# Performance work log

Measured on AMD Instinct MI355X. Metric: run time of the kernel, lower is better.

The kernel has to match this reference:

```python
import jax, jax.numpy as jnp
import numpy as np

N_HEADS = 16
ROPE_THETA = 10000.0


def setup_inputs() -> dict:
    B, T, C = 4, 2048, 2048
    hd = C // N_HEADS  # 128
    key = jax.random.key(0)
    k1, k2, k3 = jax.random.split(key, 3)
    x = jax.random.normal(k1, (B, T, C), dtype=jnp.float32)
    # RoPE frequencies: angle[t, j] = t / theta^(2j/hd)
    inv_freq = 1.0 / (ROPE_THETA ** (jnp.arange(0, hd, 2, dtype=jnp.float32) / hd))  # (hd/2,)
    angles = jnp.arange(T, dtype=jnp.float32)[:, None] * inv_freq[None, :]  # (T, hd/2)
    freqs_cos = jnp.cos(angles)
    freqs_sin = jnp.sin(angles)
    W_qkv = jax.random.normal(k2, (C, 3 * C), dtype=jnp.float32) * (C ** -0.5)
    W_out = jax.random.normal(k3, (C, C), dtype=jnp.float32) * (C ** -0.5)
    return {"x": x, "freqs_cos": freqs_cos, "freqs_sin": freqs_sin, "W_qkv": W_qkv, "W_out": W_out}


def _apply_rope(t, cos, sin):
    # t: (B, H, T, hd); cos/sin: (T, hd/2). Interleaved-pair rotation, matching
    # torch view_as_complex on reshape(..., hd/2, 2).
    hd = t.shape[-1]
    tr = t.reshape(*t.shape[:-1], hd // 2, 2)
    x0, x1 = tr[..., 0], tr[..., 1]  # (B, H, T, hd/2)
    o0 = x0 * cos - x1 * sin
    o1 = x0 * sin + x1 * cos
    return jnp.stack([o0, o1], axis=-1).reshape(t.shape)


def reference(x, freqs_cos, freqs_sin, W_qkv, W_out):
    B, T, C = x.shape
    H = N_HEADS
    hd = C // H
    qkv = x @ W_qkv  # (B, T, 3C)
    q, k, v = jnp.split(qkv, 3, axis=-1)

    def heads(t):
        return t.reshape(B, T, H, hd).transpose(0, 2, 1, 3)  # (B, H, T, hd)

    cos, sin = freqs_cos[:T], freqs_sin[:T]
    q = _apply_rope(heads(q), cos, sin)
    k = _apply_rope(heads(k), cos, sin)
    v = heads(v)

    scale = hd ** -0.5
    scores = jnp.einsum('bhqd,bhkd->bhqk', q, k) * scale  # (B, H, T, T)
    causal = jnp.tril(jnp.ones((T, T), dtype=bool))
    scores = jnp.where(causal, scores, jnp.finfo(scores.dtype).min)
    attn = jax.nn.softmax(scores, axis=-1)
    out = jnp.einsum('bhqk,bhkd->bhqd', attn, v)  # (B, H, T, hd)
    out = out.transpose(0, 2, 1, 3).reshape(B, T, C)
    return out @ W_out, k, v
```

## Files before the change

kernel.cpp:

```cpp
#include <hip/hip_runtime.h>
#include <cstdint>
#include <cstddef>

typedef __attribute__((ext_vector_type(8))) short bf16x8;
typedef __attribute__((ext_vector_type(4))) float f32x4;

__device__ __forceinline__ unsigned short f2bf(float f) {
  union { float f; unsigned u; } v; v.f = f;
  unsigned r = v.u + 0x7FFFu + ((v.u >> 16) & 1u);
  return (unsigned short)(r >> 16);
}

#define GLL(gp, lp) __builtin_amdgcn_global_load_lds( \
    (const __attribute__((address_space(1))) void*)(gp), \
    (__attribute__((address_space(3))) void*)(lp), 16, 0, 0)

#define FENCE() __builtin_amdgcn_sched_barrier(0)

__global__ void cvt_x_kernel(const float* __restrict__ x, unsigned short* __restrict__ xb, int n4) {
  int i = blockIdx.x * blockDim.x + threadIdx.x;
  if (i >= n4) return;
  const float4 v = reinterpret_cast<const float4*>(x)[i];
  ushort4 o;
  o.x = f2bf(v.x); o.y = f2bf(v.y); o.z = f2bf(v.z); o.w = f2bf(v.w);
  reinterpret_cast<ushort4*>(xb)[i] = o;
}

__global__ void transpose_kernel(const float* __restrict__ src, unsigned short* __restrict__ dst,
                                 int K, int N) {
  __shared__ float t[32][33];
  const int tx = threadIdx.x, ty = threadIdx.y;
  const int n0 = blockIdx.x * 32, k0 = blockIdx.y * 32;
#pragma unroll
  for (int i = 0; i < 4; ++i)
    t[ty + i * 8][tx] = src[(size_t)(k0 + ty + i * 8) * N + n0 + tx];
  __syncthreads();
#pragma unroll
  for (int i = 0; i < 4; ++i)
    dst[(size_t)(n0 + ty + i * 8) * K + k0 + tx] = f2bf(t[tx][ty + i * 8]);
}


template <int EPI>
__global__ void gemm2p_kernel(
    const unsigned short* __restrict__ Ag, const unsigned short* __restrict__ Bg,
    int K, int N,
    float* __restrict__ yout,
    const float* __restrict__ fcos, const float* __restrict__ fsin,
    unsigned short* __restrict__ q_ws, unsigned short* __restrict__ k_ws,
    unsigned short* __restrict__ vT_ws,
    float* __restrict__ k_out, float* __restrict__ v_out) {
  __shared__ unsigned short Asb[3][128 * 32];
  __shared__ unsigned short Bsb[3][128 * 32];

  const int tid = threadIdx.x;
  const int w = tid >> 6, lane = tid & 63;
  const int wr = w >> 1, wc = w & 1;
  const int g = lane >> 4, q16 = lane & 15;

  const int xcd = (int)blockIdx.x & 7;
  const int i = (int)blockIdx.x >> 3;
  const int bm = xcd * 8 + (i & 7);
  const int bn = i >> 3;
  const int m0 = bm << 7, n0 = bn << 7;
  const int NT = K >> 5;

  const int srow = lane >> 2;
  const int sslot = lane & 3;

  auto stageA = [&](int tile) {
    if (tile >= NT) return;
    unsigned short* dst = &Asb[tile % 3][0];
#pragma unroll
    for (int j = 0; j < 2; ++j) {
      const int row = w * 32 + j * 16 + srow;
      const int c = sslot ^ ((row >> 1) & 3);
      GLL(Ag + (size_t)(m0 + row) * K + tile * 32 + c * 8,
          dst + (w * 32 + j * 16) * 32);
    }
  };
  auto stageB = [&](int tile) {
    if (tile >= NT) return;
    unsigned short* dst = &Bsb[tile % 3][0];
#pragma unroll
    for (int j = 0; j < 2; ++j) {
      const int row = w * 32 + j * 16 + srow;
      const int c = sslot ^ ((row >> 1) & 3);
      GLL(Bg + (size_t)(n0 + row) * K + tile * 32 + c * 8,
          dst + (w * 32 + j * 16) * 32);
    }
  };

  f32x4 acc[4][4] = {};

  stageA(0); stageB(0);
  stageA(1); stageB(1);

  for (int t = 0; t < NT; ++t) {
    FENCE();
    if (t < NT - 1) { asm volatile("s_waitcnt vmcnt(4)"); }
    else            { asm volatile("s_waitcnt vmcnt(0)"); }
    FENCE();
    __builtin_amdgcn_s_barrier();
    FENCE();
    stageA(t + 2); stageB(t + 2);
    FENCE();
    const unsigned short* Ab = Asb[t % 3];
    const unsigned short* Bb = Bsb[t % 3];
    bf16x8 af[4], bfr[4];
#pragma unroll
    for (int ii = 0; ii < 4; ++ii) {
      const int row = wr * 64 + ii * 16 + q16;
      af[ii] = *(const bf16x8*)(Ab + row * 32 + ((g ^ ((row >> 1) & 3)) << 3));
    }
#pragma unroll
    for (int j = 0; j < 4; ++j) {
      const int row = wc * 64 + j * 16 + q16;
      bfr[j] = *(const bf16x8*)(Bb + row * 32 + ((g ^ ((row >> 1) & 3)) << 3));
    }
#pragma unroll
    for (int ii = 0; ii < 4; ++ii)
#pragma unroll
      for (int j = 0; j < 4; ++j)
        acc[ii][j] = __builtin_amdgcn_mfma_f32_16x16x32_bf16(af[ii], bfr[j], acc[ii][j], 0, 0, 0);
  }

#pragma unroll
  for (int ii = 0; ii < 4; ++ii) {
#pragma unroll
    for (int j = 0; j < 4; ++j) {
#pragma unroll
      for (int r = 0; r < 4; ++r) {
        const int m = m0 + wr * 64 + ii * 16 + g * 4 + r;
        const int n = n0 + wc * 64 + j * 16 + q16;
        const float val = acc[ii][j][r];
        if (EPI == 0) {
          yout[(size_t)m * N + n] = val;
        } else {
          const int region = bn >> 4;
          const int h = bn & 15;
          const int b = m >> 11, tt = m & 2047;
          const int dcol = n & 127;
          const size_t idx = ((size_t)((b * 16 + h) * 2048 + tt)) * 128 + dcol;
          if (region == 2) {
            v_out[idx] = val;
            vT_ws[((size_t)(b * 16 + h) * 128 + dcol) * 2048 + tt] = f2bf(val);
          } else {
            const int fi = dcol >> 1;
            const float c = fcos[tt * 64 + fi];
            const float s = fsin[tt * 64 + fi];
            const float part = __shfl_xor(val, 1);
            const float ro = (dcol & 1) ? (part * s + val * c) : (val * c - part * s);
            if (region == 0) {
              q_ws[idx] = f2bf(ro * 0.08838834764831845f);
            } else {
              k_out[idx] = ro;
              k_ws[idx] = f2bf(ro);
            }
          }
        }
      }
    }
  }
}

__global__ __launch_bounds__(256, 2) void attn_kernel(
    const unsigned short* __restrict__ q_ws,
    const unsigned short* __restrict__ k_ws,
    const unsigned short* __restrict__ vT_ws,
    unsigned short* __restrict__ attnout) {
  __shared__ unsigned short Kl[2][64 * 128];
  __shared__ unsigned short Vl[2][128 * 64];
  __shared__ unsigned short Pl[4][2][16 * 64];

  const int tid = threadIdx.x;
  const int w = tid >> 6, lane = tid & 63;
  const int g = lane >> 4, q16 = lane & 15;
  const int bh = blockIdx.x;
  const int qt = 15 - (int)blockIdx.y;
  const int b = bh >> 4, h = bh & 15;
  const int qbase = qt * 128;
  const int qb = qbase + w * 32;
  const size_t kvbase = (size_t)bh * 2048 * 128;

  const int krow_l = lane >> 4, kchunk = lane & 15;
  const int vrow_l = lane >> 3, vchunk = lane & 7;

  bf16x8 qf[2][4];
#pragma unroll
  for (int qs = 0; qs < 2; ++qs)
#pragma unroll
    for (int c = 0; c < 4; ++c)
      qf[qs][c] = *(const bf16x8*)&q_ws[kvbase + (size_t)(qb + qs * 16 + q16) * 128 + c * 32 + g * 8];

  f32x4 acc[2][8] = {};
  float mrun[2] = {-1e30f, -1e30f};
  float lrun[2] = {0.f, 0.f};

  const int nt = (qt + 1) * 2;

  auto stageK = [&](int buf, int kt) {
#pragma unroll
    for (int i = 0; i < 4; ++i) {
      const int slab = w * 4 + i;
      const int krow = slab * 4 + krow_l;
      GLL(k_ws + kvbase + (size_t)(kt + krow) * 128 + ((kchunk ^ (krow & 7)) << 3),
          ((unsigned short*)Kl[buf]) + slab * 512);
    }
  };
  auto stageV = [&](int buf, int kt) {
#pragma unroll
    for (int i = 0; i < 4; ++i) {
      const int slab = w * 4 + i;
      const int d = slab * 8 + vrow_l;
      GLL(vT_ws + kvbase + (size_t)d * 2048 + kt + ((vchunk ^ (d & 7)) << 3),
          ((unsigned short*)Vl[buf]) + slab * 512);
    }
  };

  stageK(0, 0); stageV(0, 0);
  int cur = 0;
  for (int it = 0; it < nt; ++it) {
    const int kt = it * 64;
    __syncthreads();
    if (it + 1 < nt) { stageK(cur ^ 1, kt + 64); stageV(cur ^ 1, kt + 64); }

    if (kt <= qb + 31) {
      f32x4 s[2][4];
#pragma unroll
      for (int qs = 0; qs < 2; ++qs)
#pragma unroll
        for (int t = 0; t < 4; ++t) s[qs][t] = f32x4{0.f, 0.f, 0.f, 0.f};
#pragma unroll
      for (int t = 0; t < 4; ++t) {
        const int key = t * 16 + q16;
#pragma unroll
        for (int c = 0; c < 4; ++c) {
          bf16x8 kf = *(const bf16x8*)&Kl[cur][key * 128 + (((c * 4 + g) ^ (key & 7)) << 3)];
          s[0][t] = __builtin_amdgcn_mfma_f32_16x16x32_bf16(kf, qf[0][c], s[0][t], 0, 0, 0);
          s[1][t] = __builtin_amdgcn_mfma_f32_16x16x32_bf16(kf, qf[1][c], s[1][t], 0, 0, 0);
        }
      }

#pragma unroll
      for (int qs = 0; qs < 2; ++qs) {
        const int qrow = qb + qs * 16 + q16;
        if (kt + 64 > qb + qs * 16) {
#pragma unroll
          for (int t = 0; t < 4; ++t)
#pragma unroll
            for (int r = 0; r < 4; ++r)
              if (kt + t * 16 + g * 4 + r > qrow) s[qs][t][r] = -1e30f;
        }
        float tm = s[qs][0][0];
#pragma unroll
        for (int t = 0; t < 4; ++t)
#pragma unroll
          for (int r = 0; r < 4; ++r) tm = fmaxf(tm, s[qs][t][r]);
        tm = fmaxf(tm, __shfl_xor(tm, 16));
        tm = fmaxf(tm, __shfl_xor(tm, 32));
        if (__any(tm > mrun[qs] + 8.0f)) {
          const float mnew = fmaxf(mrun[qs], tm);
          const float fac = __expf(mrun[qs] - mnew);
          lrun[qs] *= fac;
          mrun[qs] = mnew;
          float fr0 = __shfl(fac, g * 4 + 0), fr1 = __shfl(fac, g * 4 + 1);
          float fr2 = __shfl(fac, g * 4 + 2), fr3 = __shfl(fac, g * 4 + 3);
#pragma unroll
          for (int n = 0; n < 8; ++n) {
            acc[qs][n][0] *= fr0; acc[qs][n][1] *= fr1;
            acc[qs][n][2] *= fr2; acc[qs][n][3] *= fr3;
          }
        }
        float ps = 0.f;
        unsigned pk[8];
#pragma unroll
        for (int t = 0; t < 4; ++t) {
          const float p0 = __expf(s[qs][t][0] - mrun[qs]);
          const float p1 = __expf(s[qs][t][1] - mrun[qs]);
          const float p2 = __expf(s[qs][t][2] - mrun[qs]);
          const float p3 = __expf(s[qs][t][3] - mrun[qs]);
          ps += (p0 + p1) + (p2 + p3);
          pk[t * 2]     = (unsigned)f2bf(p0) | ((unsigned)f2bf(p1) << 16);
          pk[t * 2 + 1] = (unsigned)f2bf(p2) | ((unsigned)f2bf(p3) << 16);
        }
        ps += __shfl_xor(ps, 16);
        ps += __shfl_xor(ps, 32);
        lrun[qs] += ps;
#pragma unroll
        for (int t = 0; t < 4; ++t) {
          const unsigned byteoff = (unsigned)(q16 * 128) +
              (((unsigned)(t * 32 + g * 8)) ^ ((unsigned)(q16 & 7) << 4));
          *(uint2*)((char*)&Pl[w][qs][0] + byteoff) = make_uint2(pk[t * 2], pk[t * 2 + 1]);
        }
      }

      asm volatile("s_waitcnt lgkmcnt(0)" ::: "memory");
      __builtin_amdgcn_sched_barrier(0);
#pragma unroll
      for (int ks = 0; ks < 2; ++ks) {
        const unsigned pcol = ((unsigned)(ks * 64 + g * 16)) ^ ((unsigned)(q16 & 7) << 4);
        bf16x8 pa0 = *(const bf16x8*)((char*)&Pl[w][0][0] + q16 * 128 + pcol);
        bf16x8 pa1 = *(const bf16x8*)((char*)&Pl[w][1][0] + q16 * 128 + pcol);
#pragma unroll
        for (int n = 0; n < 8; ++n) {
          const int d = n * 16 + q16;
          bf16x8 vf = *(const bf16x8*)&Vl[cur][d * 64 + (((ks * 4 + g) ^ (d & 7)) << 3)];
          acc[0][n] = __builtin_amdgcn_mfma_f32_16x16x32_bf16(pa0, vf, acc[0][n], 0, 0, 0);
          acc[1][n] = __builtin_amdgcn_mfma_f32_16x16x32_bf16(pa1, vf, acc[1][n], 0, 0, 0);
        }
      }
    }
    cur ^= 1;
  }

#pragma unroll
  for (int qs = 0; qs < 2; ++qs) {
    float rl[4];
#pragma unroll
    for (int r = 0; r < 4; ++r) rl[r] = 1.0f / __shfl(lrun[qs], g * 4 + r);
#pragma unroll
    for (int n = 0; n < 8; ++n) {
#pragma unroll
      for (int r = 0; r < 4; ++r) {
        const int q = qb + qs * 16 + g * 4 + r;
        const int d = n * 16 + q16;
        attnout[((size_t)(b * 2048 + q)) * 2048 + h * 128 + d] = f2bf(acc[qs][n][r] * rl[r]);
      }
    }
  }
}

extern "C" void kernel_launch(void* const* d_in, const int* in_sizes, int n_in,
                              void* d_out, int out_size, void* d_ws, size_t ws_size,
                              hipStream_t stream) {
  (void)in_sizes; (void)n_in; (void)out_size; (void)ws_size;
  const float* x    = (const float*)d_in[0];
  const float* fcos = (const float*)d_in[1];
  const float* fsin = (const float*)d_in[2];
  const float* Wqkv = (const float*)d_in[3];
  const float* Wout = (const float*)d_in[4];

  float* out   = (float*)d_out;
  float* y_out = out;
  float* k_out = out + (size_t)16777216;
  float* v_out = out + (size_t)33554432;

  unsigned short* xb      = (unsigned short*)d_ws;
  unsigned short* wqkvT   = xb + 16777216;
  unsigned short* woutT   = wqkvT + 12582912;
  unsigned short* q_ws    = woutT + 4194304;
  unsigned short* k_ws    = q_ws + 16777216;
  unsigned short* vT_ws   = k_ws + 16777216;
  unsigned short* attnout = xb;

  cvt_x_kernel<<<16384, 256, 0, stream>>>(x, xb, 4194304);
  transpose_kernel<<<dim3(192, 64), dim3(32, 8), 0, stream>>>(Wqkv, wqkvT, 2048, 6144);
  transpose_kernel<<<dim3(64, 64), dim3(32, 8), 0, stream>>>(Wout, woutT, 2048, 2048);

  gemm2p_kernel<1><<<3072, 256, 0, stream>>>(
      xb, wqkvT, 2048, 6144,
      nullptr, fcos, fsin, q_ws, k_ws, vT_ws, k_out, v_out);

  attn_kernel<<<dim3(64, 16), 256, 0, stream>>>(q_ws, k_ws, vT_ws, attnout);

  gemm2p_kernel<0><<<1024, 256, 0, stream>>>(
      attnout, woutT, 2048, 2048,
      y_out, nullptr, nullptr, nullptr, nullptr, nullptr, nullptr, nullptr);
}
```

Measured before the change: 564.1 us.

## Load GEMM fragments directly from global memory into registers, dropping LDS staging

The GEMM kernel no longer stages A and B tiles through a triple-buffered shared-memory pipeline with global_load_lds and barriers. Each wave now loads its MFMA operand fragments straight from global memory into registers, double-buffered across two k-steps. This removes LDS traffic and block barriers, but it gives up the sharing of loaded tiles between waves, so global and L2 traffic rise (each A/B row is loaded by two waves) and accesses become 16-byte strided per row.

```diff
diff --git a/kernel.cpp b/kernel.cpp
--- a/kernel.cpp
+++ b/kernel.cpp
@@ -14,8 +14,6 @@
 #define GLL(gp, lp) __builtin_amdgcn_global_load_lds( \
     (const __attribute__((address_space(1))) void*)(gp), \
     (__attribute__((address_space(3))) void*)(lp), 16, 0, 0)
-
-#define FENCE() __builtin_amdgcn_sched_barrier(0)
 
 __global__ void cvt_x_kernel(const float* __restrict__ x, unsigned short* __restrict__ xb, int n4) {
   int i = blockIdx.x * blockDim.x + threadIdx.x;
@@ -42,7 +40,7 @@
 
 
 template <int EPI>
-__global__ void gemm2p_kernel(
+__global__ void gemmd_kernel(
     const unsigned short* __restrict__ Ag, const unsigned short* __restrict__ Bg,
     int K, int N,
     float* __restrict__ yout,
@@ -50,9 +48,6 @@
     unsigned short* __restrict__ q_ws, unsigned short* __restrict__ k_ws,
     unsigned short* __restrict__ vT_ws,
     float* __restrict__ k_out, float* __restrict__ v_out) {
-  __shared__ unsigned short Asb[3][128 * 32];
-  __shared__ unsigned short Bsb[3][128 * 32];
-
   const int tid = threadIdx.x;
   const int w = tid >> 6, lane = tid & 63;
   const int wr = w >> 1, wc = w & 1;
@@ -65,64 +60,46 @@
   const int m0 = bm << 7, n0 = bn << 7;
   const int NT = K >> 5;
 
-  const int srow = lane >> 2;
-  const int sslot = lane & 3;
-
-  auto stageA = [&](int tile) {
-    if (tile >= NT) return;
-    unsigned short* dst = &Asb[tile % 3][0];
-#pragma unroll
-    for (int j = 0; j < 2; ++j) {
-      const int row = w * 32 + j * 16 + srow;
-      const int c = sslot ^ ((row >> 1) & 3);
-      GLL(Ag + (size_t)(m0 + row) * K + tile * 32 + c * 8,
-          dst + (w * 32 + j * 16) * 32);
-    }
-  };
-  auto stageB = [&](int tile) {
-    if (tile >= NT) return;
-    unsigned short* dst = &Bsb[tile % 3][0];
-#pragma unroll
-    for (int j = 0; j < 2; ++j) {
-      const int row = w * 32 + j * 16 + srow;
-      const int c = sslot ^ ((row >> 1) & 3);
-      GLL(Bg + (size_t)(n0 + row) * K + tile * 32 + c * 8,
-          dst + (w * 32 + j * 16) * 32);
-    }
-  };
+  const unsigned short* pa[4];
+  const unsigned short* pb[4];
+#pragma unroll
+  for (int ii = 0; ii < 4; ++ii)
+    pa[ii] = Ag + (size_t)(m0 + wr * 64 + ii * 16 + q16) * K + g * 8;
+#pragma unroll
+  for (int j = 0; j < 4; ++j)
+    pb[j] = Bg + (size_t)(n0 + wc * 64 + j * 16 + q16) * K + g * 8;
 
   f32x4 acc[4][4] = {};
-
-  stageA(0); stageB(0);
-  stageA(1); stageB(1);
-
-  for (int t = 0; t < NT; ++t) {
-    FENCE();
-    if (t < NT - 1) { asm volatile("s_waitcnt vmcnt(4)"); }
-    else            { asm volatile("s_waitcnt vmcnt(0)"); }
-    FENCE();
-    __builtin_amdgcn_s_barrier();
-    FENCE();
-    stageA(t + 2); stageB(t + 2);
-    FENCE();
-    const unsigned short* Ab = Asb[t % 3];
-    const unsigned short* Bb = Bsb[t % 3];
-    bf16x8 af[4], bfr[4];
-#pragma unroll
-    for (int ii = 0; ii < 4; ++ii) {
-      const int row = wr * 64 + ii * 16 + q16;
-      af[ii] = *(const bf16x8*)(Ab + row * 32 + ((g ^ ((row >> 1) & 3)) << 3));
-    }
-#pragma unroll
-    for (int j = 0; j < 4; ++j) {
-      const int row = wc * 64 + j * 16 + q16;
-      bfr[j] = *(const bf16x8*)(Bb + row * 32 + ((g ^ ((row >> 1) & 3)) << 3));
-    }
+  bf16x8 a0[4], b0[4], a1[4], b1[4];
+
+#pragma unroll
+  for (int ii = 0; ii < 4; ++ii) a0[ii] = *(const bf16x8*)(pa[ii]);
+#pragma unroll
+  for (int j = 0; j < 4; ++j)  b0[j] = *(const bf16x8*)(pb[j]);
+
+  for (int t = 0; t < NT; t += 2) {
+    const int k1 = (t + 1) << 5;
+#pragma unroll
+    for (int ii = 0; ii < 4; ++ii) a1[ii] = *(const bf16x8*)(pa[ii] + k1);
+#pragma unroll
+    for (int j = 0; j < 4; ++j)  b1[j] = *(const bf16x8*)(pb[j] + k1);
 #pragma unroll
     for (int ii = 0; ii < 4; ++ii)
 #pragma unroll
       for (int j = 0; j < 4; ++j)
-        acc[ii][j] = __builtin_amdgcn_mfma_f32_16x16x32_bf16(af[ii], bfr[j], acc[ii][j], 0, 0, 0);
+        acc[ii][j] = __builtin_amdgcn_mfma_f32_16x16x32_bf16(a0[ii], b0[j], acc[ii][j], 0, 0, 0);
+    if (t + 2 < NT) {
+      const int k2 = (t + 2) << 5;
+#pragma unroll
+      for (int ii = 0; ii < 4; ++ii) a0[ii] = *(const bf16x8*)(pa[ii] + k2);
+#pragma unroll
+      for (int j = 0; j < 4; ++j)  b0[j] = *(const bf16x8*)(pb[j] + k2);
+    }
+#pragma unroll
+    for (int ii = 0; ii < 4; ++ii)
+#pragma unroll
+      for (int j = 0; j < 4; ++j)
+        acc[ii][j] = __builtin_amdgcn_mfma_f32_16x16x32_bf16(a1[ii], b1[j], acc[ii][j], 0, 0, 0);
   }
 
 #pragma unroll
@@ -358,13 +335,13 @@
   transpose_kernel<<<dim3(192, 64), dim3(32, 8), 0, stream>>>(Wqkv, wqkvT, 2048, 6144);
   transpose_kernel<<<dim3(64, 64), dim3(32, 8), 0, stream>>>(Wout, woutT, 2048, 2048);
 
-  gemm2p_kernel<1><<<3072, 256, 0, stream>>>(
+  gemmd_kernel<1><<<3072, 256, 0, stream>>>(
       xb, wqkvT, 2048, 6144,
       nullptr, fcos, fsin, q_ws, k_ws, vT_ws, k_out, v_out);
 
   attn_kernel<<<dim3(64, 16), 256, 0, stream>>>(q_ws, k_ws, vT_ws, attnout);
 
-  gemm2p_kernel<0><<<1024, 256, 0, stream>>>(
+  gemmd_kernel<0><<<1024, 256, 0, stream>>>(
       attnout, woutT, 2048, 2048,
       y_out, nullptr, nullptr, nullptr, nullptr, nullptr, nullptr, nullptr);
 }
```

Result: slower. 1.602 ms (+184.0%).
